# Optimization experiments

Measured on AMD Instinct MI355X. Metric: run time of the kernel, lower is better.

## Reference

```python
import jax, jax.numpy as jnp
import numpy as np

L_OUTPUT = 1024  # SequenceDecoder l_output


def setup_inputs() -> dict:
    key = jax.random.key(0)
    k1, k2, k3 = jax.random.split(key, 3)
    B, L, D, DO = 16, 4096, 1024, 1024
    x = jax.random.normal(k1, (B, L, D), dtype=jnp.float32)
    # 0/1 padding-style mask; valid_length = mask.sum(axis=1)
    attention_mask = jax.random.randint(k2, (B, L), 0, 2, dtype=jnp.int32)
    # nn.Linear(d_model, d_output): weight (DO, D), bias (DO,)
    W = jax.random.normal(k3, (DO, D), dtype=jnp.float32) * (1.0 / np.sqrt(D))
    b = jnp.zeros((DO,), dtype=jnp.float32)
    return {"x": x, "attention_mask": attention_mask, "W": W, "b": b}


def _restrict_last(x, attention_mask, l_output):
    """Vectorized equivalent of the per-sample Python loop in mode='last':
    for each batch row i, take the LAST s_i = min(valid_len_i, l_output)
    elements of the full sequence, zero-padded at the tail to l_output.
    (When all s_i == l_output this matches x[:, -l_output:, :], which is the
    only case the original torch.stack-based loop handles without error.)"""
    B, L, D = x.shape
    valid = attention_mask.sum(axis=1)                    # (B,)
    s = jnp.minimum(valid, l_output)                      # (B,)
    j = jnp.arange(l_output)                              # (l_output,)
    idx = jnp.clip(L - s[:, None] + j[None, :], 0, L - 1) # (B, l_output)
    gathered = jnp.take_along_axis(x, idx[:, :, None], axis=1)  # (B, l_output, D)
    keep = (j[None, :] < s[:, None])[:, :, None]          # (B, l_output, 1)
    return jnp.where(keep, gathered, jnp.zeros((), dtype=x.dtype))


def reference(x, attention_mask, W, b):
    # mode='last' restrict, then output_transform = nn.Linear(d_model, d_output)
    restricted = _restrict_last(x, attention_mask, L_OUTPUT)  # (B, l_output, D)
    return jnp.einsum('bld,od->blo', restricted, W) + b       # (B, l_output, DO)
```

## Files before the change

### kernel.cpp

```cpp
#include <hip/hip_runtime.h>
#include <hip/hip_bf16.h>

#define L_SEQ   4096
#define D_IN    1024
#define N_BATCH 16
#define L_OUT   1024
#define D_OUT   1024
#define M_DIM   (N_BATCH * L_OUT)
#define K_DIM   D_IN

#define BM 256
#define BN 256
#define BK 32
#define NKT (K_DIM / BK)

typedef __attribute__((ext_vector_type(4))) float  f32x4;
typedef __attribute__((ext_vector_type(8))) __bf16 bf16x8;
typedef __attribute__((ext_vector_type(4))) __bf16 bf16x4;

#define WS_W_OFF 0u
#define WS_S_OFF (4u * 1024u * 1024u)

__global__ __launch_bounds__(256) void prep_kernel(
    const int*   __restrict__ mask,
    const float* __restrict__ W,
    int*    __restrict__ s_out,
    __bf16* __restrict__ wsW)
{
    const int t = threadIdx.x;
    if (blockIdx.x < 16) {
        const int b = blockIdx.x;
        const int* row = mask + (size_t)b * L_SEQ;
        int sum = 0;
#pragma unroll
        for (int i = 0; i < L_SEQ / 256; ++i) sum += row[t + i * 256];
#pragma unroll
        for (int off = 32; off > 0; off >>= 1) sum += __shfl_down(sum, off, 64);
        __shared__ int wsum[4];
        if ((t & 63) == 0) wsum[t >> 6] = sum;
        __syncthreads();
        if (t == 0) {
            int total = wsum[0] + wsum[1] + wsum[2] + wsum[3];
            s_out[b] = total < L_OUT ? total : L_OUT;
        }
    } else {
        const int n  = blockIdx.x - 16;
        const int e0 = t * 4;
        const int sl   = (e0 >> 3) & 3;
        const int dste = (e0 & ~31) | ((sl ^ ((n >> 1) & 3)) << 3) | (e0 & 7);
        const float* src = W + (size_t)n * D_IN + e0;
        f32x4 v = *(const f32x4*)src;
        bf16x4 o = {(__bf16)v.x, (__bf16)v.y, (__bf16)v.z, (__bf16)v.w};
        *(bf16x4*)(wsW + (size_t)n * K_DIM + dste) = o;
    }
}

__device__ __forceinline__ void gload16v(const void* g, void* l) {
    __builtin_amdgcn_global_load_lds(
        (const __attribute__((address_space(1))) void*)g,
        (__attribute__((address_space(3))) void*)l,
        16, 0, 0);
}

#define FENCE() asm volatile("" ::: "memory")

__global__ __launch_bounds__(512, 2) void gemm_kernel(
    const float*  __restrict__ x,
    const __bf16* __restrict__ Wb,
    const float*  __restrict__ bias,
    const int*    __restrict__ s_arr,
    float* __restrict__ out)
{
    __shared__ float  sAf[3][BM * BK];
    __shared__ __bf16 sB [2][BN * BK];

    const int t  = threadIdx.x;
    const int bx = blockIdx.x;
    const int vb = (bx & 7) * 32 + (bx >> 3);
    const int tile_n = vb & 3;
    const int tile_m = vb >> 2;
    const int m0 = tile_m * BM;
    const int n0 = tile_n * BN;
    const int lane = t & 63;
    const int wave = t >> 6;
    const int wm = wave >> 2;
    const int wn = wave & 3;

    const int bb = m0 >> 10;
    const int s  = s_arr[bb];
    const int jb = m0 & (L_OUT - 1);
    const float* xb = x + (size_t)bb * L_SEQ * D_IN;
    const int ascol = (((t & 7) ^ ((t >> 3) & 7)) * 4);
    const float* asrc[4];
    int  adst[4];
    int  arow[4];
#pragma unroll
    for (int r = 0; r < 4; ++r) {
        const int rr = 64 * r + (t >> 3);
        const int j  = jb + rr;
        const int xr = (j < s) ? (L_SEQ - s + j) : 0;
        asrc[r] = xb + (size_t)xr * D_IN + ascol;
        adst[r] = rr * BK + (t & 7) * 4;
        arow[r] = j;
    }
#define STAGE_A(abuf, kt_)                                                 \
    {                                                                      \
        _Pragma("unroll")                                                  \
        for (int r = 0; r < 4; ++r)                                        \
            gload16v(asrc[r] + (kt_) * BK, (abuf) + adst[r]);              \
    }

    const __bf16* Bg = Wb + (size_t)n0 * K_DIM;
    const int brow = t >> 2;
    const int bcol = (t & 3) * 8;
#define STAGE_B(buf, kt_)                                                  \
    {                                                                      \
        _Pragma("unroll")                                                  \
        for (int r = 0; r < 2; ++r) {                                      \
            const int row_ = 128 * r + brow;                               \
            gload16v(Bg + (size_t)row_ * K_DIM + (kt_) * BK + bcol,        \
                     &sB[buf][row_ * BK + bcol]);                          \
        }                                                                  \
    }

    const int fr = lane & 15;
    const int g4 = lane >> 4;

    float bias_v[4];
#pragma unroll
    for (int gg = 0; gg < 4; ++gg)
        bias_v[gg] = bias[n0 + wn * 64 + gg * 16 + fr];

    bf16x8 aF[4], bB0[2], bB1[2];
    f32x4 acc[8][4];
#pragma unroll
    for (int f = 0; f < 8; ++f)
#pragma unroll
        for (int gg = 0; gg < 4; ++gg) acc[f][gg] = (f32x4){0.f, 0.f, 0.f, 0.f};

#define LOAD_A32(abuf, mh)                                                 \
    {                                                                      \
        _Pragma("unroll")                                                  \
        for (int i = 0; i < 4; ++i) {                                      \
            const int R_ = wm * 128 + (mh) * 64 + i * 16 + fr;             \
            const float* rbase_ = (abuf) + R_ * BK;                        \
            f32x4 lo_ = *(const f32x4*)&rbase_[((2*g4)   ^ (R_ & 7)) * 4]; \
            f32x4 hi_ = *(const f32x4*)&rbase_[((2*g4+1) ^ (R_ & 7)) * 4]; \
            aF[i] = (bf16x8){(__bf16)lo_.x, (__bf16)lo_.y, (__bf16)lo_.z,  \
                             (__bf16)lo_.w, (__bf16)hi_.x, (__bf16)hi_.y,  \
                             (__bf16)hi_.z, (__bf16)hi_.w};                \
        }                                                                  \
    }

#define LOAD_B(buf, nh, BB)                                                \
    {                                                                      \
        _Pragma("unroll")                                                  \
        for (int j = 0; j < 2; ++j) {                                      \
            const int RB_ = wn * 64 + (nh) * 32 + j * 16 + fr;             \
            BB[j] = *(const bf16x8*)                                       \
                &sB[buf][RB_ * BK + (g4 ^ ((RB_ >> 1) & 3)) * 8];          \
        }                                                                  \
    }

#define MFMA8(mh, nh, BB)                                                  \
    {                                                                      \
        _Pragma("unroll")                                                  \
        for (int i = 0; i < 4; ++i)                                        \
            _Pragma("unroll")                                              \
            for (int j = 0; j < 2; ++j)                                    \
                acc[(mh) * 4 + i][(nh) * 2 + j] =                          \
                    __builtin_amdgcn_mfma_f32_16x16x32_bf16(               \
                        aF[i], BB[j], acc[(mh) * 4 + i][(nh) * 2 + j],     \
                        0, 0, 0);                                          \
    }

    float* a0 = &sAf[0][0];
    float* a1 = &sAf[1][0];
    float* a2 = &sAf[2][0];

    STAGE_A(a0, 0);
    STAGE_B(0, 0);
    STAGE_A(a1, 1);

    for (int kt = 0; kt < NKT; ++kt) {
        const int cur = kt & 1;
        const int nxt = cur ^ 1;

        FENCE();
        if (kt == NKT - 1) asm volatile("s_waitcnt vmcnt(0)" ::: "memory");
        else               asm volatile("s_waitcnt vmcnt(4)" ::: "memory");
        __builtin_amdgcn_s_barrier();
        FENCE();
        if (s < L_OUT) {
#pragma unroll
            for (int r = 0; r < 4; ++r)
                if (arow[r] >= s)
                    *(f32x4*)&a0[adst[r]] = (f32x4){0.f, 0.f, 0.f, 0.f};
            __syncthreads();
        }
        LOAD_A32(a0, 0);
        LOAD_B(cur, 0, bB0);
        LOAD_B(cur, 1, bB1);
        if (kt + 1 < NKT) STAGE_B(nxt, kt + 1);
        __builtin_amdgcn_s_setprio(1);
        MFMA8(0, 0, bB0);
        MFMA8(0, 1, bB1);
        __builtin_amdgcn_s_setprio(0);

        FENCE();
        __builtin_amdgcn_s_barrier();
        FENCE();
        LOAD_A32(a0, 1);
        if (kt + 2 < NKT) STAGE_A(a2, kt + 2);
        __builtin_amdgcn_s_setprio(1);
        MFMA8(1, 1, bB1);
        MFMA8(1, 0, bB0);
        __builtin_amdgcn_s_setprio(0);

        float* ta = a0; a0 = a1; a1 = a2; a2 = ta;
    }

    const int row0 = m0 + wm * 128 + (lane >> 4) * 4;
    const int col0 = n0 + wn * 64 + fr;
#pragma unroll
    for (int f = 0; f < 8; ++f)
#pragma unroll
        for (int gg = 0; gg < 4; ++gg)
#pragma unroll
            for (int rr = 0; rr < 4; ++rr)
                out[(size_t)(row0 + f * 16 + rr) * D_OUT + (col0 + gg * 16)] =
                    acc[f][gg][rr] + bias_v[gg];

#undef STAGE_A
#undef STAGE_B
#undef LOAD_A32
#undef LOAD_B
#undef MFMA8
}

extern "C" void kernel_launch(void* const* d_in, const int* in_sizes, int n_in,
                              void* d_out, int out_size, void* d_ws, size_t ws_size,
                              hipStream_t stream) {
    const float* x    = (const float*)d_in[0];
    const int*   mask = (const int*)d_in[1];
    const float* W    = (const float*)d_in[2];
    const float* bias = (const float*)d_in[3];
    float*       out  = (float*)d_out;

    __bf16* wsW   = (__bf16*)((char*)d_ws + WS_W_OFF);
    int*    s_arr = (int*)((char*)d_ws + WS_S_OFF);

    prep_kernel<<<dim3(16 + D_OUT), dim3(256), 0, stream>>>(
        mask, W, s_arr, wsW);

    const int grid = (M_DIM / BM) * (D_OUT / BN);
    gemm_kernel<<<dim3(grid), dim3(512), 0, stream>>>(
        x, wsW, bias, s_arr, out);
}
```

Baseline: 55.99 us.

## Remap wave tiling to 4x2 layout so A fragments load once per k-step

Changes the per-wave sub-tile from 128x64 (2x4 waves) to 64x128 (4x2 waves). Each wave now loads its A fragments from LDS, converting fp32 to bf16, only once per k-tile instead of twice, and loads B in two groups of four. This cuts the A conversion work and LDS reads for A, at the cost of more B fragment reads. The two-phase barrier schedule is restructured to match: the second phase now loads the upper B half instead of the second A half.

```diff
diff --git a/kernel.cpp b/kernel.cpp
--- a/kernel.cpp
+++ b/kernel.cpp
@@ -83,8 +83,8 @@
     const int n0 = tile_n * BN;
     const int lane = t & 63;
     const int wave = t >> 6;
-    const int wm = wave >> 2;
-    const int wn = wave & 3;
+    const int wm = wave & 3;
+    const int wn = wave >> 2;
 
     const int bb = m0 >> 10;
     const int s  = s_arr[bb];
@@ -126,23 +126,23 @@
     const int fr = lane & 15;
     const int g4 = lane >> 4;
 
-    float bias_v[4];
-#pragma unroll
-    for (int gg = 0; gg < 4; ++gg)
-        bias_v[gg] = bias[n0 + wn * 64 + gg * 16 + fr];
-
-    bf16x8 aF[4], bB0[2], bB1[2];
-    f32x4 acc[8][4];
-#pragma unroll
-    for (int f = 0; f < 8; ++f)
-#pragma unroll
-        for (int gg = 0; gg < 4; ++gg) acc[f][gg] = (f32x4){0.f, 0.f, 0.f, 0.f};
-
-#define LOAD_A32(abuf, mh)                                                 \
+    float bias_v[8];
+#pragma unroll
+    for (int q = 0; q < 8; ++q)
+        bias_v[q] = bias[n0 + wn * 128 + q * 16 + fr];
+
+    bf16x8 aF[4], bBlo[4], bBhi[4];
+    f32x4 acc[4][8];
+#pragma unroll
+    for (int i = 0; i < 4; ++i)
+#pragma unroll
+        for (int q = 0; q < 8; ++q) acc[i][q] = (f32x4){0.f, 0.f, 0.f, 0.f};
+
+#define LOAD_A32(abuf)                                                     \
     {                                                                      \
         _Pragma("unroll")                                                  \
         for (int i = 0; i < 4; ++i) {                                      \
-            const int R_ = wm * 128 + (mh) * 64 + i * 16 + fr;             \
+            const int R_ = wm * 64 + i * 16 + fr;                          \
             const float* rbase_ = (abuf) + R_ * BK;                        \
             f32x4 lo_ = *(const f32x4*)&rbase_[((2*g4)   ^ (R_ & 7)) * 4]; \
             f32x4 hi_ = *(const f32x4*)&rbase_[((2*g4+1) ^ (R_ & 7)) * 4]; \
@@ -152,26 +152,25 @@
         }                                                                  \
     }
 
-#define LOAD_B(buf, nh, BB)                                                \
-    {                                                                      \
-        _Pragma("unroll")                                                  \
-        for (int j = 0; j < 2; ++j) {                                      \
-            const int RB_ = wn * 64 + (nh) * 32 + j * 16 + fr;             \
+#define LOAD_B4(buf, qb, BB)                                               \
+    {                                                                      \
+        _Pragma("unroll")                                                  \
+        for (int j = 0; j < 4; ++j) {                                      \
+            const int RB_ = wn * 128 + ((qb) + j) * 16 + fr;               \
             BB[j] = *(const bf16x8*)                                       \
                 &sB[buf][RB_ * BK + (g4 ^ ((RB_ >> 1) & 3)) * 8];          \
         }                                                                  \
     }
 
-#define MFMA8(mh, nh, BB)                                                  \
+#define MFMA16(qb, BB)                                                     \
     {                                                                      \
         _Pragma("unroll")                                                  \
         for (int i = 0; i < 4; ++i)                                        \
             _Pragma("unroll")                                              \
-            for (int j = 0; j < 2; ++j)                                    \
-                acc[(mh) * 4 + i][(nh) * 2 + j] =                          \
+            for (int j = 0; j < 4; ++j)                                    \
+                acc[i][(qb) + j] =                                         \
                     __builtin_amdgcn_mfma_f32_16x16x32_bf16(               \
-                        aF[i], BB[j], acc[(mh) * 4 + i][(nh) * 2 + j],     \
-                        0, 0, 0);                                          \
+                        aF[i], BB[j], acc[i][(qb) + j], 0, 0, 0);          \
     }
 
     float* a0 = &sAf[0][0];
@@ -198,44 +197,41 @@
                     *(f32x4*)&a0[adst[r]] = (f32x4){0.f, 0.f, 0.f, 0.f};
             __syncthreads();
         }
-        LOAD_A32(a0, 0);
-        LOAD_B(cur, 0, bB0);
-        LOAD_B(cur, 1, bB1);
+        LOAD_A32(a0);
+        LOAD_B4(cur, 0, bBlo);
         if (kt + 1 < NKT) STAGE_B(nxt, kt + 1);
         __builtin_amdgcn_s_setprio(1);
-        MFMA8(0, 0, bB0);
-        MFMA8(0, 1, bB1);
+        MFMA16(0, bBlo);
         __builtin_amdgcn_s_setprio(0);
 
         FENCE();
         __builtin_amdgcn_s_barrier();
         FENCE();
-        LOAD_A32(a0, 1);
+        LOAD_B4(cur, 4, bBhi);
         if (kt + 2 < NKT) STAGE_A(a2, kt + 2);
         __builtin_amdgcn_s_setprio(1);
-        MFMA8(1, 1, bB1);
-        MFMA8(1, 0, bB0);
+        MFMA16(4, bBhi);
         __builtin_amdgcn_s_setprio(0);
 
         float* ta = a0; a0 = a1; a1 = a2; a2 = ta;
     }
 
-    const int row0 = m0 + wm * 128 + (lane >> 4) * 4;
-    const int col0 = n0 + wn * 64 + fr;
-#pragma unroll
-    for (int f = 0; f < 8; ++f)
-#pragma unroll
-        for (int gg = 0; gg < 4; ++gg)
+    const int row0 = m0 + wm * 64 + (lane >> 4) * 4;
+    const int col0 = n0 + wn * 128 + fr;
+#pragma unroll
+    for (int i = 0; i < 4; ++i)
+#pragma unroll
+        for (int q = 0; q < 8; ++q)
 #pragma unroll
             for (int rr = 0; rr < 4; ++rr)
-                out[(size_t)(row0 + f * 16 + rr) * D_OUT + (col0 + gg * 16)] =
-                    acc[f][gg][rr] + bias_v[gg];
+                out[(size_t)(row0 + i * 16 + rr) * D_OUT + (col0 + q * 16)] =
+                    acc[i][q][rr] + bias_v[q];
 
 #undef STAGE_A
 #undef STAGE_B
 #undef LOAD_A32
-#undef LOAD_B
-#undef MFMA8
+#undef LOAD_B4
+#undef MFMA16
 }
 
 extern "C" void kernel_launch(void* const* d_in, const int* in_sizes, int n_in,
```

New measurement: 51.79 us. -7.5%, faster.
